# Optimization experiments

Hardware: AMD Instinct MI355X
Metric: run time of the kernel (lower is better)

Reference implementation:

```python
import jax, jax.numpy as jnp
import numpy as np

B = 65536
D = 1280   # input_dim (ESM2-650M pooled feature dim)
H = 512    # hidden_dim
T = 4      # number of affinity types (Kd, Ki, IC50, EC50)


def setup_inputs() -> dict:
    key = jax.random.key(0)
    ks = jax.random.split(key, 6)
    features = jax.random.normal(ks[0], (B, D), dtype=jnp.float32)
    affinity_type_idx = jax.random.randint(ks[1], (B,), 0, T, dtype=jnp.int32)
    # Per-type head parameters (stacked over the T heads).
    s1 = 1.0 / np.sqrt(D)
    s2 = 1.0 / np.sqrt(H)
    W1 = jax.random.uniform(ks[2], (T, D, H), jnp.float32, -s1, s1)
    b1 = jax.random.uniform(ks[3], (T, H), jnp.float32, -s1, s1)
    w2 = jax.random.uniform(ks[4], (T, H), jnp.float32, -s2, s2)  # Linear(H,1) weight, squeezed
    b2 = jax.random.uniform(ks[5], (T,), jnp.float32, -s2, s2)
    return {"features": features, "affinity_type_idx": affinity_type_idx,
            "W1": W1, "b1": b1, "w2": w2, "b2": b2}


def reference(features, affinity_type_idx, W1, b1, w2, b2):
    # Compute every head for every sample (T is tiny), then select the routed one.
    # h: (B, T, H)
    h = jnp.einsum('bd,tdh->bth', features, W1) + b1
    h = jax.nn.gelu(h, approximate=False)  # torch nn.GELU default = exact erf GELU
    # preds_all: (B, T) — each head's Linear(H, 1) output, squeezed
    preds_all = jnp.einsum('bth,th->bt', h, w2) + b2
    # Route: pick each sample's own affinity-type head.
    preds = jnp.take_along_axis(preds_all, affinity_type_idx[:, None].astype(jnp.int32), axis=1)
    return preds[:, 0]  # (B,)
```

## Files before the change

kernel.cpp:

```cpp
#include <hip/hip_runtime.h>
#include <math.h>

#define NB 65536
#define ND 1280
#define NH 512
#define NT 4

typedef float f32x4 __attribute__((ext_vector_type(4)));
typedef float f32x2 __attribute__((ext_vector_type(2)));
typedef short s16x8 __attribute__((ext_vector_type(8)));
typedef unsigned int u32x2 __attribute__((ext_vector_type(2)));
typedef unsigned int u32x4 __attribute__((ext_vector_type(4)));
typedef unsigned long long ull;
typedef unsigned short u16;

static __device__ __forceinline__ unsigned f2bf1(float x) {
    union { float f; unsigned u; } v; v.f = x;
    return (v.u + 0x7fffu + ((v.u >> 16) & 1u)) >> 16;
}
static __device__ __forceinline__ unsigned packbf(float a, float b) {
    return f2bf1(a) | (f2bf1(b) << 16);
}
static __device__ __forceinline__ int swz(int a) {
    return a ^ (((a >> 7) & 7) << 4);
}
static __device__ __forceinline__ float gelu_exact(float x) {
    return 0.5f * x * (1.0f + erff(x * 0.70710678118654752f));
}
static __device__ __forceinline__ void gload_lds16(const void* g, void* l) {
    __builtin_amdgcn_global_load_lds(
        (const __attribute__((address_space(1))) unsigned int*)g,
        (__attribute__((address_space(3))) unsigned int*)l, 16, 0, 0);
}

__global__ __launch_bounds__(256) void transpose_kernel(const float* __restrict__ W1,
                                                        u16* __restrict__ Wt) {
    __shared__ float tile[64][65];
    int b = blockIdx.x;
    int dt = b % 20; int r = b / 20; int ht = r & 7; int t = r >> 3;
    int d0 = dt * 64, h0 = ht * 64;
    int tid = threadIdx.x;
    const float* src = W1 + ((size_t)t * ND + d0) * NH + h0;
#pragma unroll
    for (int it = 0; it < 16; ++it) {
        int dl = it * 4 + (tid >> 6);
        tile[dl][tid & 63] = src[(size_t)dl * NH + (tid & 63)];
    }
    __syncthreads();
    int hl = tid >> 2, ds = (tid & 3) * 16;
    unsigned pk[8];
#pragma unroll
    for (int j = 0; j < 8; ++j)
        pk[j] = packbf(tile[ds + 2 * j][hl], tile[ds + 2 * j + 1][hl]);
    u16* dst = Wt + ((size_t)(t * NH + h0 + hl)) * ND + d0 + ds;
    *(u32x4*)dst = (u32x4){pk[0], pk[1], pk[2], pk[3]};
    *(u32x4*)(dst + 8) = (u32x4){pk[4], pk[5], pk[6], pk[7]};
}

__global__ __launch_bounds__(256) void count_kernel(const int* __restrict__ idx,
                                                    int* __restrict__ bc) {
    int tid = threadIdx.x;
    int i = blockIdx.x * 256 + tid;
    int t = idx[i];
    int lane = tid & 63, wave = tid >> 6;
    ull b0 = __ballot(t & 1);
    ull b1 = __ballot(t & 2);
    ull mask = ((t & 1) ? b0 : ~b0) & ((t & 2) ? b1 : ~b1);
    int rank = __popcll(mask & ((1ULL << lane) - 1ULL));
    __shared__ int lc[4][4];
    if (tid < 16) ((int*)lc)[tid] = 0;
    __syncthreads();
    if (rank == 0) lc[wave][t] = __popcll(mask);
    __syncthreads();
    if (tid < 4)
        bc[blockIdx.x * 4 + tid] = lc[0][tid] + lc[1][tid] + lc[2][tid] + lc[3][tid];
}

__global__ __launch_bounds__(64) void scan_kernel(const int* __restrict__ bc,
        int* __restrict__ counts, int* __restrict__ base) {
    __shared__ int tot[4];
    int t = threadIdx.x;
    if (t < 4) {
        int s = 0;
        for (int b = 0; b < 256; ++b) s += bc[b * 4 + t];
        tot[t] = s;
        counts[t] = s;
    }
    __syncthreads();
    if (t < 4) {
        int run = 0;
        for (int u = 0; u < t; ++u) run += tot[u];
        for (int b = 0; b < 256; ++b) {
            base[b * 4 + t] = run;
            run += bc[b * 4 + t];
        }
    }
}

__global__ __launch_bounds__(256) void scatter_kernel(const int* __restrict__ idx,
        const int* __restrict__ base, int* __restrict__ perm,
        const float* __restrict__ b2, float* __restrict__ out) {
    int tid = threadIdx.x;
    int i = blockIdx.x * 256 + tid;
    int t = idx[i];
    int lane = tid & 63, wave = tid >> 6;
    ull b0 = __ballot(t & 1);
    ull b1 = __ballot(t & 2);
    ull mask = ((t & 1) ? b0 : ~b0) & ((t & 2) ? b1 : ~b1);
    int rank = __popcll(mask & ((1ULL << lane) - 1ULL));
    __shared__ int lc[4][4];
    if (tid < 16) ((int*)lc)[tid] = 0;
    __syncthreads();
    if (rank == 0) lc[wave][t] = __popcll(mask);
    __syncthreads();
    int pre = 0;
#pragma unroll
    for (int w = 0; w < 4; ++w) pre += (w < wave) ? lc[w][t] : 0;
    perm[base[blockIdx.x * 4 + t] + pre + rank] = i;
    out[i] = b2[t];
}

template<int USEWT>
__global__ __launch_bounds__(256, 3) void gemm_kernel(
        const float* __restrict__ feat, const float* __restrict__ W1,
        const u16* __restrict__ Wt,
        const float* __restrict__ b1, const float* __restrict__ w2,
        const int* __restrict__ perm, const int* __restrict__ counts,
        float* __restrict__ partials, float* __restrict__ out, int use_partials) {
    __shared__ char smem[32768];

    int bx = blockIdx.x;
    int r8 = bx & 7, m8 = bx >> 3;
    int ct = m8 & 3, q = m8 >> 2;
    int g = q * 8 + r8;
    int t = g >> 9, tile_m = g & 511;
    int cnt = counts[t];
    int tilebase = tile_m * 128;
    if (tilebase >= cnt) return;
    int off_t = 0;
    for (int u = 0; u < t; ++u) off_t += counts[u];

    int tid = threadIdx.x;
    int lane = tid & 63, wave = tid >> 6;
    int wr = wave >> 1, wc = wave & 1;
    int hc0 = ct * 128;

    unsigned aoff[8];
#pragma unroll
    for (int i = 0; i < 8; ++i) {
        int r = tilebase + i * 16 + (tid >> 4);
        if (r > cnt - 1) r = cnt - 1;
        int s = perm[off_t + r];
        aoff[i] = (unsigned)s * ND + (tid & 15) * 4;
    }

    f32x4 acc[4][4];
#pragma unroll
    for (int a = 0; a < 4; ++a)
#pragma unroll
        for (int b = 0; b < 4; ++b) acc[a][b] = (f32x4){0.f, 0.f, 0.f, 0.f};

    f32x4 apf[8];

    auto LOADA = [&](int k0) {
#pragma unroll
        for (int i = 0; i < 8; ++i)
            apf[i] = *(const f32x4*)(feat + aoff[i] + k0);
    };
    auto WRITEA = [&]() {
#pragma unroll
        for (int i = 0; i < 8; ++i) {
            int row = i * 16 + (tid >> 4);
            u32x2 v;
            v.x = packbf(apf[i][0], apf[i][1]);
            v.y = packbf(apf[i][2], apf[i][3]);
            *(u32x2*)(smem + swz(row * 128 + (tid & 15) * 8)) = v;
        }
    };
    auto COMPUTE_KS = [&](int ks) {
        int kbyte = ks * 64 + (lane >> 4) * 16;
        s16x8 af[4], bf[4];
#pragma unroll
        for (int f = 0; f < 4; ++f) {
            int rowA = wr * 64 + f * 16 + (lane & 15);
            af[f] = *(const s16x8*)(smem + swz(rowA * 128 + kbyte));
            int colB = wc * 64 + f * 16 + (lane & 15);
            bf[f] = *(const s16x8*)(smem + 16384 + swz(colB * 128 + kbyte));
        }
#pragma unroll
        for (int fm = 0; fm < 4; ++fm)
#pragma unroll
            for (int fn = 0; fn < 4; ++fn)
                acc[fm][fn] = __builtin_amdgcn_mfma_f32_16x16x32_bf16(
                    af[fm], bf[fn], acc[fm][fn], 0, 0, 0);
    };

    if constexpr (USEWT) {
        unsigned boff[4];
#pragma unroll
        for (int j = 0; j < 4; ++j) {
            int a = wave * 4096 + j * 1024 + lane * 16;
            int col = a >> 7, chunk = (a >> 4) & 7;
            boff[j] = (unsigned)((t * NH + hc0 + col) * ND + ((chunk ^ (col & 7)) * 8));
        }
        auto STAGE_B = [&](int kt) {
#pragma unroll
            for (int j = 0; j < 4; ++j)
                gload_lds16(Wt + boff[j] + kt * 64,
                            smem + 16384 + wave * 4096 + j * 1024);
        };
        LOADA(0);
        STAGE_B(0);
        WRITEA();
        __syncthreads();
#pragma unroll 1
        for (int kt = 0; kt < 20; ++kt) {
            if (kt < 19) LOADA((kt + 1) * 64);
            COMPUTE_KS(0);
            COMPUTE_KS(1);
            __syncthreads();
            if (kt < 19) {
                STAGE_B(kt + 1);
                WRITEA();
                __syncthreads();
            }
        }
    } else {
        int cpair = (tid & 63) * 2;
        int kkbase = tid >> 6;
        const float* wbase = W1 + (size_t)t * ND * NH + hc0 + cpair;
        f32x2 bpf[4][4];
        auto LOADB = [&](int k0) {
#pragma unroll
            for (int qq = 0; qq < 4; ++qq) {
                int d = k0 + (kkbase + qq * 4) * 4;
#pragma unroll
                for (int e = 0; e < 4; ++e)
                    bpf[qq][e] = *(const f32x2*)(wbase + (size_t)(d + e) * NH);
            }
        };
        auto WRITEB = [&]() {
#pragma unroll
            for (int qq = 0; qq < 4; ++qq) {
                int kk = kkbase + qq * 4;
#pragma unroll
                for (int j = 0; j < 2; ++j) {
                    u32x2 v;
                    v.x = packbf(bpf[qq][0][j], bpf[qq][1][j]);
                    v.y = packbf(bpf[qq][2][j], bpf[qq][3][j]);
                    *(u32x2*)(smem + 16384 + swz((cpair + j) * 128 + kk * 8)) = v;
                }
            }
        };
        LOADA(0); LOADB(0);
        WRITEA(); WRITEB();
        __syncthreads();
#pragma unroll 1
        for (int kt = 0; kt < 20; ++kt) {
            bool nxt = (kt + 1 < 20);
            if (nxt) LOADA((kt + 1) * 64);
            COMPUTE_KS(0);
            if (nxt) LOADB((kt + 1) * 64);
            COMPUTE_KS(1);
            if (nxt) {
                __syncthreads();
                WRITEA(); WRITEB();
                __syncthreads();
            }
        }
    }

    float part[4][4];
#pragma unroll
    for (int fm = 0; fm < 4; ++fm)
#pragma unroll
        for (int r = 0; r < 4; ++r) part[fm][r] = 0.f;
#pragma unroll
    for (int fn = 0; fn < 4; ++fn) {
        int h = hc0 + wc * 64 + fn * 16 + (lane & 15);
        float b1v = b1[t * NH + h];
        float w2v = w2[t * NH + h];
#pragma unroll
        for (int fm = 0; fm < 4; ++fm)
#pragma unroll
            for (int r = 0; r < 4; ++r) {
                float v = acc[fm][fn][r] + b1v;
                part[fm][r] += gelu_exact(v) * w2v;
            }
    }
#pragma unroll
    for (int m = 1; m <= 8; m <<= 1)
#pragma unroll
        for (int fm = 0; fm < 4; ++fm)
#pragma unroll
            for (int r = 0; r < 4; ++r)
                part[fm][r] += __shfl_xor(part[fm][r], m, 64);

    if ((lane & 15) == 0) {
        int slot = ct * 2 + wc;
#pragma unroll
        for (int fm = 0; fm < 4; ++fm)
#pragma unroll
            for (int r = 0; r < 4; ++r) {
                int row = wr * 64 + fm * 16 + (lane >> 4) * 4 + r;
                int gr = tilebase + row;
                if (gr < cnt) {
                    int s = perm[off_t + gr];
                    if (use_partials)
                        partials[(size_t)s * 8 + slot] = part[fm][r];
                    else
                        atomicAdd(&out[s], part[fm][r]);
                }
            }
    }
}

__global__ __launch_bounds__(256) void reduce_kernel(const float* __restrict__ partials,
        const int* __restrict__ idx, const float* __restrict__ b2,
        float* __restrict__ out) {
    int i = blockIdx.x * 256 + threadIdx.x;
    const float* p = partials + (size_t)i * 8;
    float s = b2[idx[i]];
#pragma unroll
    for (int j = 0; j < 8; ++j) s += p[j];
    out[i] = s;
}

extern "C" void kernel_launch(void* const* d_in, const int* in_sizes, int n_in,
                              void* d_out, int out_size, void* d_ws, size_t ws_size,
                              hipStream_t stream) {
    (void)in_sizes; (void)n_in; (void)out_size;
    const float* feat = (const float*)d_in[0];
    const int*   idx  = (const int*)d_in[1];
    const float* W1   = (const float*)d_in[2];
    const float* b1   = (const float*)d_in[3];
    const float* w2   = (const float*)d_in[4];
    const float* b2   = (const float*)d_in[5];
    float* out = (float*)d_out;

    char* ws = (char*)d_ws;
    int* counts  = (int*)ws;
    int* bc      = (int*)(ws + 64);
    int* base    = (int*)(ws + 64 + 4096);
    int* perm    = (int*)(ws + 64 + 8192);
    float* partials = (float*)(ws + 64 + 8192 + (size_t)NB * 4);
    u16* Wt = (u16*)(ws + 64 + 8192 + (size_t)NB * 4 + (size_t)NB * 32);
    size_t need_part = 64 + 8192 + (size_t)NB * 4 + (size_t)NB * 32;
    size_t need_full = need_part + (size_t)NT * ND * NH * 2;
    int use_partials = (ws_size >= need_part) ? 1 : 0;
    int use_wt = (ws_size >= need_full) ? 1 : 0;

    if (use_wt)
        transpose_kernel<<<NT * 8 * 20, 256, 0, stream>>>(W1, Wt);
    count_kernel<<<NB / 256, 256, 0, stream>>>(idx, bc);
    scan_kernel<<<1, 64, 0, stream>>>(bc, counts, base);
    scatter_kernel<<<NB / 256, 256, 0, stream>>>(idx, base, perm, b2, out);
    if (use_wt)
        gemm_kernel<1><<<8192, 256, 0, stream>>>(feat, W1, Wt, b1, w2, perm, counts,
                                                 partials, out, use_partials);
    else
        gemm_kernel<0><<<8192, 256, 0, stream>>>(feat, W1, Wt, b1, w2, perm, counts,
                                                 partials, out, use_partials);
    if (use_partials)
        reduce_kernel<<<NB / 256, 256, 0, stream>>>(partials, idx, b2, out);
}
```

Measured before the change: 229.2 us.

## Load MFMA operands straight from global memory, bypassing LDS staging

The main GEMM path no longer stages A and B tiles through shared memory. Each wave loads its own fp32 feature fragments and pre-transposed bf16 weight fragments directly into registers in MFMA operand layout, converts A to bf16 in registers, and runs a 40-step loop with no barriers, prefetching the next A chunk. This removes LDS writes, reads and __syncthreads, but each wave now fetches its operands itself, so global and L2 traffic goes up and there is no cross-wave reuse through LDS. The older LDS-based path is kept as a separate fallback kernel.

```diff
diff --git a/kernel.cpp b/kernel.cpp
--- a/kernel.cpp
+++ b/kernel.cpp
@@ -21,16 +21,14 @@
 static __device__ __forceinline__ unsigned packbf(float a, float b) {
     return f2bf1(a) | (f2bf1(b) << 16);
 }
+static __device__ __forceinline__ s16x8 as_s16x8(u32x4 v) {
+    union { u32x4 u; s16x8 s; } x; x.u = v; return x.s;
+}
 static __device__ __forceinline__ int swz(int a) {
     return a ^ (((a >> 7) & 7) << 4);
 }
 static __device__ __forceinline__ float gelu_exact(float x) {
     return 0.5f * x * (1.0f + erff(x * 0.70710678118654752f));
-}
-static __device__ __forceinline__ void gload_lds16(const void* g, void* l) {
-    __builtin_amdgcn_global_load_lds(
-        (const __attribute__((address_space(1))) unsigned int*)g,
-        (__attribute__((address_space(3))) unsigned int*)l, 16, 0, 0);
 }
 
 __global__ __launch_bounds__(256) void transpose_kernel(const float* __restrict__ W1,
@@ -120,15 +118,11 @@
     out[i] = b2[t];
 }
 
-template<int USEWT>
-__global__ __launch_bounds__(256, 3) void gemm_kernel(
-        const float* __restrict__ feat, const float* __restrict__ W1,
-        const u16* __restrict__ Wt,
+__global__ __launch_bounds__(256, 3) void gemm_direct(
+        const float* __restrict__ feat, const u16* __restrict__ Wt,
         const float* __restrict__ b1, const float* __restrict__ w2,
         const int* __restrict__ perm, const int* __restrict__ counts,
         float* __restrict__ partials, float* __restrict__ out, int use_partials) {
-    __shared__ char smem[32768];
-
     int bx = blockIdx.x;
     int r8 = bx & 7, m8 = bx >> 3;
     int ct = m8 & 3, q = m8 >> 2;
@@ -143,15 +137,17 @@
     int tid = threadIdx.x;
     int lane = tid & 63, wave = tid >> 6;
     int wr = wave >> 1, wc = wave & 1;
-    int hc0 = ct * 128;
-
-    unsigned aoff[8];
-#pragma unroll
-    for (int i = 0; i < 8; ++i) {
-        int r = tilebase + i * 16 + (tid >> 4);
+    int hc0 = ct * 128 + wc * 64;
+    int rl = lane & 15;
+    int kl = (lane >> 4) * 8;
+
+    unsigned aoff[4], boff[4];
+#pragma unroll
+    for (int f = 0; f < 4; ++f) {
+        int r = tilebase + wr * 64 + f * 16 + rl;
         if (r > cnt - 1) r = cnt - 1;
-        int s = perm[off_t + r];
-        aoff[i] = (unsigned)s * ND + (tid & 15) * 4;
+        aoff[f] = (unsigned)perm[off_t + r] * ND + kl;
+        boff[f] = (unsigned)(t * NH + hc0 + f * 16 + rl) * ND + kl;
     }
 
     f32x4 acc[4][4];
@@ -160,114 +156,47 @@
 #pragma unroll
         for (int b = 0; b < 4; ++b) acc[a][b] = (f32x4){0.f, 0.f, 0.f, 0.f};
 
-    f32x4 apf[8];
-
-    auto LOADA = [&](int k0) {
-#pragma unroll
-        for (int i = 0; i < 8; ++i)
-            apf[i] = *(const f32x4*)(feat + aoff[i] + k0);
-    };
-    auto WRITEA = [&]() {
-#pragma unroll
-        for (int i = 0; i < 8; ++i) {
-            int row = i * 16 + (tid >> 4);
-            u32x2 v;
-            v.x = packbf(apf[i][0], apf[i][1]);
-            v.y = packbf(apf[i][2], apf[i][3]);
-            *(u32x2*)(smem + swz(row * 128 + (tid & 15) * 8)) = v;
-        }
-    };
-    auto COMPUTE_KS = [&](int ks) {
-        int kbyte = ks * 64 + (lane >> 4) * 16;
-        s16x8 af[4], bf[4];
+    f32x4 apf[4][2];
+    u32x4 abf[4];
+    s16x8 bfr[4];
+
+    auto LOADA = [&](int kt) {
 #pragma unroll
         for (int f = 0; f < 4; ++f) {
-            int rowA = wr * 64 + f * 16 + (lane & 15);
-            af[f] = *(const s16x8*)(smem + swz(rowA * 128 + kbyte));
-            int colB = wc * 64 + f * 16 + (lane & 15);
-            bf[f] = *(const s16x8*)(smem + 16384 + swz(colB * 128 + kbyte));
-        }
+            const float* p = feat + aoff[f] + kt * 32;
+            apf[f][0] = *(const f32x4*)p;
+            apf[f][1] = *(const f32x4*)(p + 4);
+        }
+    };
+    auto LOADB = [&](int kt) {
+#pragma unroll
+        for (int f = 0; f < 4; ++f)
+            bfr[f] = *(const s16x8*)(Wt + boff[f] + kt * 32);
+    };
+    auto CVT = [&]() {
+#pragma unroll
+        for (int f = 0; f < 4; ++f)
+            abf[f] = (u32x4){packbf(apf[f][0][0], apf[f][0][1]),
+                             packbf(apf[f][0][2], apf[f][0][3]),
+                             packbf(apf[f][1][0], apf[f][1][1]),
+                             packbf(apf[f][1][2], apf[f][1][3])};
+    };
+    auto MFMA = [&]() {
 #pragma unroll
         for (int fm = 0; fm < 4; ++fm)
 #pragma unroll
             for (int fn = 0; fn < 4; ++fn)
                 acc[fm][fn] = __builtin_amdgcn_mfma_f32_16x16x32_bf16(
-                    af[fm], bf[fn], acc[fm][fn], 0, 0, 0);
-    };
-
-    if constexpr (USEWT) {
-        unsigned boff[4];
-#pragma unroll
-        for (int j = 0; j < 4; ++j) {
-            int a = wave * 4096 + j * 1024 + lane * 16;
-            int col = a >> 7, chunk = (a >> 4) & 7;
-            boff[j] = (unsigned)((t * NH + hc0 + col) * ND + ((chunk ^ (col & 7)) * 8));
-        }
-        auto STAGE_B = [&](int kt) {
-#pragma unroll
-            for (int j = 0; j < 4; ++j)
-                gload_lds16(Wt + boff[j] + kt * 64,
-                            smem + 16384 + wave * 4096 + j * 1024);
-        };
-        LOADA(0);
-        STAGE_B(0);
-        WRITEA();
-        __syncthreads();
+                    as_s16x8(abf[fm]), bfr[fn], acc[fm][fn], 0, 0, 0);
+    };
+
+    LOADA(0);
 #pragma unroll 1
-        for (int kt = 0; kt < 20; ++kt) {
-            if (kt < 19) LOADA((kt + 1) * 64);
-            COMPUTE_KS(0);
-            COMPUTE_KS(1);
-            __syncthreads();
-            if (kt < 19) {
-                STAGE_B(kt + 1);
-                WRITEA();
-                __syncthreads();
-            }
-        }
-    } else {
-        int cpair = (tid & 63) * 2;
-        int kkbase = tid >> 6;
-        const float* wbase = W1 + (size_t)t * ND * NH + hc0 + cpair;
-        f32x2 bpf[4][4];
-        auto LOADB = [&](int k0) {
-#pragma unroll
-            for (int qq = 0; qq < 4; ++qq) {
-                int d = k0 + (kkbase + qq * 4) * 4;
-#pragma unroll
-                for (int e = 0; e < 4; ++e)
-                    bpf[qq][e] = *(const f32x2*)(wbase + (size_t)(d + e) * NH);
-            }
-        };
-        auto WRITEB = [&]() {
-#pragma unroll
-            for (int qq = 0; qq < 4; ++qq) {
-                int kk = kkbase + qq * 4;
-#pragma unroll
-                for (int j = 0; j < 2; ++j) {
-                    u32x2 v;
-                    v.x = packbf(bpf[qq][0][j], bpf[qq][1][j]);
-                    v.y = packbf(bpf[qq][2][j], bpf[qq][3][j]);
-                    *(u32x2*)(smem + 16384 + swz((cpair + j) * 128 + kk * 8)) = v;
-                }
-            }
-        };
-        LOADA(0); LOADB(0);
-        WRITEA(); WRITEB();
-        __syncthreads();
-#pragma unroll 1
-        for (int kt = 0; kt < 20; ++kt) {
-            bool nxt = (kt + 1 < 20);
-            if (nxt) LOADA((kt + 1) * 64);
-            COMPUTE_KS(0);
-            if (nxt) LOADB((kt + 1) * 64);
-            COMPUTE_KS(1);
-            if (nxt) {
-                __syncthreads();
-                WRITEA(); WRITEB();
-                __syncthreads();
-            }
-        }
+    for (int kt = 0; kt < 40; ++kt) {
+        LOADB(kt);
+        CVT();
+        if (kt < 39) LOADA(kt + 1);
+        MFMA();
     }
 
     float part[4][4];
@@ -277,7 +206,7 @@
         for (int r = 0; r < 4; ++r) part[fm][r] = 0.f;
 #pragma unroll
     for (int fn = 0; fn < 4; ++fn) {
-        int h = hc0 + wc * 64 + fn * 16 + (lane & 15);
+        int h = hc0 + fn * 16 + rl;
         float b1v = b1[t * NH + h];
         float w2v = w2[t * NH + h];
 #pragma unroll
@@ -296,7 +225,7 @@
             for (int r = 0; r < 4; ++r)
                 part[fm][r] += __shfl_xor(part[fm][r], m, 64);
 
-    if ((lane & 15) == 0) {
+    if (rl == 0) {
         int slot = ct * 2 + wc;
 #pragma unroll
         for (int fm = 0; fm < 4; ++fm)
@@ -315,6 +244,160 @@
     }
 }
 
+__global__ __launch_bounds__(256, 2) void gemm_fallback(
+        const float* __restrict__ feat, const float* __restrict__ W1,
+        const float* __restrict__ b1, const float* __restrict__ w2,
+        const int* __restrict__ perm, const int* __restrict__ counts,
+        float* __restrict__ partials, float* __restrict__ out, int use_partials) {
+    __shared__ char smem[32768];
+    int bx = blockIdx.x;
+    int r8 = bx & 7, m8 = bx >> 3;
+    int ct = m8 & 3, q = m8 >> 2;
+    int g = q * 8 + r8;
+    int t = g >> 9, tile_m = g & 511;
+    int cnt = counts[t];
+    int tilebase = tile_m * 128;
+    if (tilebase >= cnt) return;
+    int off_t = 0;
+    for (int u = 0; u < t; ++u) off_t += counts[u];
+
+    int tid = threadIdx.x;
+    int lane = tid & 63, wave = tid >> 6;
+    int wr = wave >> 1, wc = wave & 1;
+    int hc0 = ct * 128;
+
+    unsigned aoff[8];
+#pragma unroll
+    for (int i = 0; i < 8; ++i) {
+        int r = tilebase + i * 16 + (tid >> 4);
+        if (r > cnt - 1) r = cnt - 1;
+        int s = perm[off_t + r];
+        aoff[i] = (unsigned)s * ND + (tid & 15) * 4;
+    }
+    f32x4 acc[4][4];
+#pragma unroll
+    for (int a = 0; a < 4; ++a)
+#pragma unroll
+        for (int b = 0; b < 4; ++b) acc[a][b] = (f32x4){0.f, 0.f, 0.f, 0.f};
+    f32x4 apf[8];
+    int cpair = (tid & 63) * 2;
+    int kkbase = tid >> 6;
+    const float* wbase = W1 + (size_t)t * ND * NH + hc0 + cpair;
+    f32x2 bpf[4][4];
+    auto LOADA = [&](int k0) {
+#pragma unroll
+        for (int i = 0; i < 8; ++i)
+            apf[i] = *(const f32x4*)(feat + aoff[i] + k0);
+    };
+    auto LOADB = [&](int k0) {
+#pragma unroll
+        for (int qq = 0; qq < 4; ++qq) {
+            int d = k0 + (kkbase + qq * 4) * 4;
+#pragma unroll
+            for (int e = 0; e < 4; ++e)
+                bpf[qq][e] = *(const f32x2*)(wbase + (size_t)(d + e) * NH);
+        }
+    };
+    auto WRITEA = [&]() {
+#pragma unroll
+        for (int i = 0; i < 8; ++i) {
+            int row = i * 16 + (tid >> 4);
+            u32x2 v;
+            v.x = packbf(apf[i][0], apf[i][1]);
+            v.y = packbf(apf[i][2], apf[i][3]);
+            *(u32x2*)(smem + swz(row * 128 + (tid & 15) * 8)) = v;
+        }
+    };
+    auto WRITEB = [&]() {
+#pragma unroll
+        for (int qq = 0; qq < 4; ++qq) {
+            int kk = kkbase + qq * 4;
+#pragma unroll
+            for (int j = 0; j < 2; ++j) {
+                u32x2 v;
+                v.x = packbf(bpf[qq][0][j], bpf[qq][1][j]);
+                v.y = packbf(bpf[qq][2][j], bpf[qq][3][j]);
+                *(u32x2*)(smem + 16384 + swz((cpair + j) * 128 + kk * 8)) = v;
+            }
+        }
+    };
+    auto COMPUTE_KS = [&](int ks) {
+        int kbyte = ks * 64 + (lane >> 4) * 16;
+        s16x8 af[4], bf[4];
+#pragma unroll
+        for (int f = 0; f < 4; ++f) {
+            int rowA = wr * 64 + f * 16 + (lane & 15);
+            af[f] = *(const s16x8*)(smem + swz(rowA * 128 + kbyte));
+            int colB = wc * 64 + f * 16 + (lane & 15);
+            bf[f] = *(const s16x8*)(smem + 16384 + swz(colB * 128 + kbyte));
+        }
+#pragma unroll
+        for (int fm = 0; fm < 4; ++fm)
+#pragma unroll
+            for (int fn = 0; fn < 4; ++fn)
+                acc[fm][fn] = __builtin_amdgcn_mfma_f32_16x16x32_bf16(
+                    af[fm], bf[fn], acc[fm][fn], 0, 0, 0);
+    };
+    LOADA(0); LOADB(0);
+    WRITEA(); WRITEB();
+    __syncthreads();
+#pragma unroll 1
+    for (int kt = 0; kt < 20; ++kt) {
+        bool nxt = (kt + 1 < 20);
+        if (nxt) LOADA((kt + 1) * 64);
+        COMPUTE_KS(0);
+        if (nxt) LOADB((kt + 1) * 64);
+        COMPUTE_KS(1);
+        if (nxt) {
+            __syncthreads();
+            WRITEA(); WRITEB();
+            __syncthreads();
+        }
+    }
+    float part[4][4];
+#pragma unroll
+    for (int fm = 0; fm < 4; ++fm)
+#pragma unroll
+        for (int r = 0; r < 4; ++r) part[fm][r] = 0.f;
+#pragma unroll
+    for (int fn = 0; fn < 4; ++fn) {
+        int h = hc0 + wc * 64 + fn * 16 + (lane & 15);
+        float b1v = b1[t * NH + h];
+        float w2v = w2[t * NH + h];
+#pragma unroll
+        for (int fm = 0; fm < 4; ++fm)
+#pragma unroll
+            for (int r = 0; r < 4; ++r) {
+                float v = acc[fm][fn][r] + b1v;
+                part[fm][r] += gelu_exact(v) * w2v;
+            }
+    }
+#pragma unroll
+    for (int m = 1; m <= 8; m <<= 1)
+#pragma unroll
+        for (int fm = 0; fm < 4; ++fm)
+#pragma unroll
+            for (int r = 0; r < 4; ++r)
+                part[fm][r] += __shfl_xor(part[fm][r], m, 64);
+    if ((lane & 15) == 0) {
+        int slot = ct * 2 + wc;
+#pragma unroll
+        for (int fm = 0; fm < 4; ++fm)
+#pragma unroll
+            for (int r = 0; r < 4; ++r) {
+                int row = wr * 64 + fm * 16 + (lane >> 4) * 4 + r;
+                int gr = tilebase + row;
+                if (gr < cnt) {
+                    int s = perm[off_t + gr];
+                    if (use_partials)
+                        partials[(size_t)s * 8 + slot] = part[fm][r];
+                    else
+                        atomicAdd(&out[s], part[fm][r]);
+                }
+            }
+    }
+}
+
 __global__ __launch_bounds__(256) void reduce_kernel(const float* __restrict__ partials,
         const int* __restrict__ idx, const float* __restrict__ b2,
         float* __restrict__ out) {
@@ -356,11 +439,11 @@
     scan_kernel<<<1, 64, 0, stream>>>(bc, counts, base);
     scatter_kernel<<<NB / 256, 256, 0, stream>>>(idx, base, perm, b2, out);
     if (use_wt)
-        gemm_kernel<1><<<8192, 256, 0, stream>>>(feat, W1, Wt, b1, w2, perm, counts,
-                                                 partials, out, use_partials);
+        gemm_direct<<<8192, 256, 0, stream>>>(feat, Wt, b1, w2, perm, counts,
+                                              partials, out, use_partials);
     else
-        gemm_kernel<0><<<8192, 256, 0, stream>>>(feat, W1, Wt, b1, w2, perm, counts,
-                                                 partials, out, use_partials);
+        gemm_fallback<<<8192, 256, 0, stream>>>(feat, W1, b1, w2, perm, counts,
+                                                partials, out, use_partials);
     if (use_partials)
         reduce_kernel<<<NB / 256, 256, 0, stream>>>(partials, idx, b2, out);
 }
```

Result: slower. 548.0 us (+139.1%).
